# Kernel optimization log

Measured on AMD Instinct MI355X. Metric: run time of the kernel, lower is better.

Reference implementation:

```python
import jax, jax.numpy as jnp
import numpy as np

LATENT_PACKET_SIZE = 16

def setup_inputs() -> dict:
    key = jax.random.key(0)
    z = jax.random.normal(key, (4096, 1, 8192), dtype=jnp.float32)
    return {"z": z}

def reference(z) -> jnp.ndarray:
    B = z.shape[0]
    D = z.shape[2]
    P = LATENT_PACKET_SIZE
    n_packets = D // P
    zp = z.reshape(B, n_packets, P)                      # (B, N, P)
    # sort packets within each sample by the first element of each packet
    inds = jnp.argsort(zp[:, :, 0], axis=1)              # (B, N) int
    z_ordered = jnp.take_along_axis(zp, inds[:, :, None], axis=1)  # batched gather
    return z_ordered.reshape(B, 1, n_packets * P)
```

## Files before the change

kernel.cpp:

```cpp
#include <hip/hip_runtime.h>


#define NPK 512
#define DIM 8192
#define NT  512

typedef float vfloat4 __attribute__((ext_vector_type(4)));

__device__ __forceinline__ unsigned long long shfl_xor_u64(unsigned long long v, int mask) {
    const int lo = __shfl_xor((int)(unsigned int)(v & 0xffffffffull), mask);
    const int hi = __shfl_xor((int)(unsigned int)(v >> 32), mask);
    return ((unsigned long long)(unsigned int)hi << 32) | (unsigned int)lo;
}

__global__ __launch_bounds__(NT, 8)
void sort_latent_kernel(const float* __restrict__ z, float* __restrict__ out) {
    __shared__ __align__(16) unsigned long long keys[NPK];
    __shared__ int srcs[NPK];

    const int t = threadIdx.x;
    const size_t rowoff = (size_t)blockIdx.x * DIM;
    const float* __restrict__ zrow = z + rowoff;
    const vfloat4* __restrict__ zin4 = (const vfloat4*)zrow;
    vfloat4* __restrict__ out4 = (vfloat4*)(out + rowoff);

    unsigned int u = __float_as_uint(zrow[t * 16]);
    if (u == 0x80000000u) u = 0u;
    u = (u & 0x80000000u) ? ~u : (u | 0x80000000u);
    unsigned long long v = ((unsigned long long)u << 16) | (unsigned long long)t;

#pragma unroll
    for (int kk = 1; kk <= 9; ++kk) {
        const int k = 1 << kk;
#pragma unroll
        for (int jj = kk - 1; jj >= 0; --jj) {
            const int j = 1 << jj;
            unsigned long long vp;
            if (j < 64) {
                vp = shfl_xor_u64(v, j);
            } else {
                __syncthreads();
                keys[t] = v;
                __syncthreads();
                vp = keys[t ^ j];
            }
            const bool take_min = (((t & k) == 0) == ((t & j) == 0));
            const bool lt = (v < vp);
            v = (take_min == lt) ? v : vp;
        }
    }

    srcs[t] = (int)(v & 0xffffull);
    __syncthreads();

#pragma unroll
    for (int i = 0; i < DIM / 4 / NT; ++i) {
        const int o = t + NT * i;
        const int src = srcs[o >> 2];
        const vfloat4 val = zin4[(src << 2) | (o & 3)];
        __builtin_nontemporal_store(val, &out4[o]);
    }
}

extern "C" void kernel_launch(void* const* d_in, const int* in_sizes, int n_in,
                              void* d_out, int out_size, void* d_ws, size_t ws_size,
                              hipStream_t stream) {
    const float* z = (const float*)d_in[0];
    float* out = (float*)d_out;
    const int nrows = in_sizes[0] / DIM;
    sort_latent_kernel<<<nrows, NT, 0, stream>>>(z, out);
}
```

Measured before the change: 232.1 us.

## Sort each row within one wavefront using register bitonic plus DPP swizzles

Each wavefront now sorts a whole row of 512 keys, eight keys per lane, so no block barriers or LDS exchanges are needed. Stages with strides under 8 become in-register compare-swaps. Cross-lane stages use DPP or ds_swizzle where possible instead of generic shuffles. Four rows share a 256-thread block. This costs more registers per thread and leaves fewer lanes issuing the gather loads per row.

```diff
diff --git a/kernel.cpp b/kernel.cpp
--- a/kernel.cpp
+++ b/kernel.cpp
@@ -3,31 +3,47 @@
 
 #define NPK 512
 #define DIM 8192
-#define NT  512
+#define NT  256
+#define RPB 4
 
 typedef float vfloat4 __attribute__((ext_vector_type(4)));
 
-__device__ __forceinline__ unsigned long long shfl_xor_u64(unsigned long long v, int mask) {
-    const int lo = __shfl_xor((int)(unsigned int)(v & 0xffffffffull), mask);
-    const int hi = __shfl_xor((int)(unsigned int)(v >> 32), mask);
-    return ((unsigned long long)(unsigned int)hi << 32) | (unsigned int)lo;
+__device__ __forceinline__ unsigned int sx32(unsigned int x, int lj) {
+    if (lj == 1)  return (unsigned int)__builtin_amdgcn_mov_dpp((int)x, 0xB1, 0xF, 0xF, true);
+    if (lj == 2)  return (unsigned int)__builtin_amdgcn_mov_dpp((int)x, 0x4E, 0xF, 0xF, true);
+    if (lj == 4)  return (unsigned int)__builtin_amdgcn_ds_swizzle((int)x, 0x101F);
+    if (lj == 8)  return (unsigned int)__builtin_amdgcn_ds_swizzle((int)x, 0x201F);
+    if (lj == 16) return (unsigned int)__builtin_amdgcn_ds_swizzle((int)x, 0x401F);
+    return (unsigned int)__shfl_xor((int)x, lj);
+}
+
+__device__ __forceinline__ unsigned long long sx64(unsigned long long v, int lj) {
+    const unsigned int lo = sx32((unsigned int)v, lj);
+    const unsigned int hi = sx32((unsigned int)(v >> 32), lj);
+    return ((unsigned long long)hi << 32) | lo;
 }
 
 __global__ __launch_bounds__(NT, 8)
 void sort_latent_kernel(const float* __restrict__ z, float* __restrict__ out) {
-    __shared__ __align__(16) unsigned long long keys[NPK];
-    __shared__ int srcs[NPK];
+    __shared__ int srcs[RPB][NPK];
 
-    const int t = threadIdx.x;
-    const size_t rowoff = (size_t)blockIdx.x * DIM;
-    const float* __restrict__ zrow = z + rowoff;
+    const int t    = threadIdx.x;
+    const int w    = t >> 6;
+    const int lane = t & 63;
+    const size_t rowoff = ((size_t)blockIdx.x * RPB + w) * DIM;
+    const float*  __restrict__ zrow = z + rowoff;
     const vfloat4* __restrict__ zin4 = (const vfloat4*)zrow;
     vfloat4* __restrict__ out4 = (vfloat4*)(out + rowoff);
 
-    unsigned int u = __float_as_uint(zrow[t * 16]);
-    if (u == 0x80000000u) u = 0u;
-    u = (u & 0x80000000u) ? ~u : (u | 0x80000000u);
-    unsigned long long v = ((unsigned long long)u << 16) | (unsigned long long)t;
+    unsigned long long v[8];
+#pragma unroll
+    for (int s = 0; s < 8; ++s) {
+        const int e = lane * 8 + s;
+        unsigned int u = __float_as_uint(zrow[e * 16]);
+        if (u == 0x80000000u) u = 0u;
+        u = (u & 0x80000000u) ? ~u : (u | 0x80000000u);
+        v[s] = ((unsigned long long)u << 16) | (unsigned long long)e;
+    }
 
 #pragma unroll
     for (int kk = 1; kk <= 9; ++kk) {
@@ -35,29 +51,43 @@
 #pragma unroll
         for (int jj = kk - 1; jj >= 0; --jj) {
             const int j = 1 << jj;
-            unsigned long long vp;
-            if (j < 64) {
-                vp = shfl_xor_u64(v, j);
+            if (j >= 8) {
+                const int lj = j >> 3;
+                const bool up = ((lane & (k >> 3)) == 0);
+                const bool keep_min = (up == ((lane & lj) == 0));
+#pragma unroll
+                for (int s = 0; s < 8; ++s) {
+                    const unsigned long long a  = v[s];
+                    const unsigned long long vp = sx64(a, lj);
+                    const bool lt = a < vp;
+                    v[s] = (keep_min == lt) ? a : vp;
+                }
             } else {
-                __syncthreads();
-                keys[t] = v;
-                __syncthreads();
-                vp = keys[t ^ j];
+#pragma unroll
+                for (int s = 0; s < 8; ++s) {
+                    if ((s & j) == 0) {
+                        const int p = s | j;
+                        const bool up = ((((lane << 3) | s) & k) == 0);
+                        const unsigned long long a = v[s], b = v[p];
+                        const bool lt = a < b;
+                        const bool do_swap = (lt != up);
+                        v[s] = do_swap ? b : a;
+                        v[p] = do_swap ? a : b;
+                    }
+                }
             }
-            const bool take_min = (((t & k) == 0) == ((t & j) == 0));
-            const bool lt = (v < vp);
-            v = (take_min == lt) ? v : vp;
         }
     }
 
-    srcs[t] = (int)(v & 0xffffull);
-    __syncthreads();
+#pragma unroll
+    for (int s = 0; s < 8; ++s)
+        srcs[w][lane * 8 + s] = (int)(v[s] & 0xffffull);
 
-#pragma unroll
-    for (int i = 0; i < DIM / 4 / NT; ++i) {
-        const int o = t + NT * i;
-        const int src = srcs[o >> 2];
-        const vfloat4 val = zin4[(src << 2) | (o & 3)];
+#pragma unroll 8
+    for (int i = 0; i < DIM / 4 / 64; ++i) {
+        const int o = i * 64 + lane;
+        const int src = srcs[w][o >> 2];
+        const vfloat4 val = zin4[src * 4 + (o & 3)];
         __builtin_nontemporal_store(val, &out4[o]);
     }
 }
@@ -68,5 +98,5 @@
     const float* z = (const float*)d_in[0];
     float* out = (float*)d_out;
     const int nrows = in_sizes[0] / DIM;
-    sort_latent_kernel<<<nrows, NT, 0, stream>>>(z, out);
+    sort_latent_kernel<<<nrows / RPB, NT, 0, stream>>>(z, out);
 }
```

Measured after the change: 254.6 us. 9.7% more time.
